# Optimization experiments

Measured on AMD Instinct MI355X. Metric: run time of the kernel, lower is better.

## Reference

```python
import jax, jax.numpy as jnp
import numpy as np

HIDDEN = 1024
NHEAD = 16
HEAD_DIM = HIDDEN // NHEAD
B, S = 2, 2048


def setup_inputs() -> dict:
    key = jax.random.key(0)
    ks = jax.random.split(key, 10)
    scale = 1.0 / np.sqrt(HIDDEN)
    inp = {
        "x": jax.random.normal(ks[0], (B, S, HIDDEN), dtype=jnp.float32),
        "mask": jax.random.randint(ks[1], (B, S), 0, 2).astype(bool),
        "Wq": jax.random.normal(ks[2], (HIDDEN, HIDDEN), dtype=jnp.float32) * scale,
        "bq": jnp.zeros((HIDDEN,), dtype=jnp.float32),
        "Wk": jax.random.normal(ks[3], (HIDDEN, HIDDEN), dtype=jnp.float32) * scale,
        "bk": jnp.zeros((HIDDEN,), dtype=jnp.float32),
        "Wv": jax.random.normal(ks[4], (HIDDEN, HIDDEN), dtype=jnp.float32) * scale,
        "bv": jnp.zeros((HIDDEN,), dtype=jnp.float32),
        "Wo": jax.random.normal(ks[5], (HIDDEN, HIDDEN), dtype=jnp.float32) * scale,
        "bo": jnp.zeros((HIDDEN,), dtype=jnp.float32),
    }
    return inp


def reference(x, mask, Wq, bq, Wk, bk, Wv, bv, Wo, bo):
    B_, S_, H = x.shape
    # QKV projections (torch Linear: x @ W.T + b), split into heads -> [B, nhead, S, head_dim]
    def split_heads(t):
        return t.reshape(B_, S_, NHEAD, HEAD_DIM).transpose(0, 2, 1, 3)

    q = split_heads(x @ Wq.T + bq)
    k = split_heads(x @ Wk.T + bk)
    v = split_heads(x @ Wv.T + bv)

    # scaled dot-product scores: [B, nhead, S, S]
    energy = jnp.einsum("bhqd,bhkd->bhqk", q, k) / jnp.sqrt(jnp.float32(HEAD_DIM))

    # combined padding + diagonal-exclusion mask: mask keys where mask[b,k] is True,
    # but never mask the diagonal (self) position
    eye = jnp.eye(S_, dtype=bool)  # [S, S]
    attn_mask = mask[:, None, None, :] & ~eye[None, None, :, :]  # [B, 1, S, S] broadcast over heads
    energy = jnp.where(attn_mask, -jnp.inf, energy)

    attention = jax.nn.softmax(energy, axis=-1)
    out = jnp.einsum("bhqk,bhkd->bhqd", attention, v)  # [B, nhead, S, head_dim]
    out = out.transpose(0, 2, 1, 3).reshape(B_, S_, H)
    return out @ Wo.T + bo
```

## Files before the change

kernel.cpp:

```cpp
#include <hip/hip_runtime.h>

typedef __attribute__((ext_vector_type(8))) short short8;
typedef __attribute__((ext_vector_type(4))) float f32x4;
typedef __attribute__((ext_vector_type(16))) float f32x16;
typedef __attribute__((ext_vector_type(4))) unsigned short ushort4v;

#define HIDDEN 1024
#define NHEAD 16
#define HD 64
#define BATCH 2
#define SEQ 2048
#define MROWS (BATCH * SEQ)
#define QSCALE 0.18033688011112042f

__device__ __forceinline__ unsigned short f2b(float f) {
  union { float f; unsigned u; } v; v.f = f;
  unsigned r = v.u + 0x7fffu + ((v.u >> 16) & 1u);
  return (unsigned short)(r >> 16);
}

__device__ __forceinline__ unsigned cvt_pk_bf16(float lo, float hi) {
  unsigned r;
  asm("v_cvt_pk_bf16_f32 %0, %1, %2" : "=v"(r) : "v"(lo), "v"(hi));
  return r;
}

__device__ __forceinline__ float fexp2(float x) {
#if __has_builtin(__builtin_amdgcn_exp2f)
  return __builtin_amdgcn_exp2f(x);
#else
  return exp2f(x);
#endif
}

__device__ __forceinline__ void gll16(const void* g, void* l) {
  __builtin_amdgcn_global_load_lds(
      (__attribute__((address_space(1))) void*)g,
      (__attribute__((address_space(3))) void*)l, 16, 0, 0);
}

__global__ void prep_kernel(const float* __restrict__ x,
                            const float* __restrict__ Wq,
                            const float* __restrict__ Wk,
                            const float* __restrict__ Wv,
                            const float* __restrict__ Wo,
                            unsigned short* __restrict__ xb,
                            unsigned short* __restrict__ wqb,
                            unsigned short* __restrict__ wkb,
                            unsigned short* __restrict__ wvb,
                            unsigned short* __restrict__ wob) {
  int bid = blockIdx.x;
  const float* src;
  unsigned short* dst;
  int base;
  if (bid < 4096)      { src = x;  dst = xb;  base = bid; }
  else if (bid < 5120) { src = Wq; dst = wqb; base = bid - 4096; }
  else if (bid < 6144) { src = Wk; dst = wkb; base = bid - 5120; }
  else if (bid < 7168) { src = Wv; dst = wvb; base = bid - 6144; }
  else                 { src = Wo; dst = wob; base = bid - 7168; }
  int i = (base * 256 + threadIdx.x) * 4;
  float4 v = *reinterpret_cast<const float4*>(src + i);
  ushort4v o;
  o.x = f2b(v.x); o.y = f2b(v.y); o.z = f2b(v.z); o.w = f2b(v.w);
  *reinterpret_cast<ushort4v*>(dst + i) = o;
}

__global__ void amask_kernel(const int* __restrict__ m, float* __restrict__ am,
                             int n) {
  int i = blockIdx.x * blockDim.x + threadIdx.x;
  if (i < n) am[i] = m[i] ? -1e30f : 0.f;
}

__global__ __launch_bounds__(256) void gemm_qkv_kernel(
    const unsigned short* __restrict__ A,
    const unsigned short* __restrict__ W0,
    const unsigned short* __restrict__ W1,
    const unsigned short* __restrict__ W2,
    const float* __restrict__ c0, const float* __restrict__ c1,
    const float* __restrict__ c2, void* __restrict__ o0,
    void* __restrict__ o1, void* __restrict__ o2) {
  __shared__ __align__(16) unsigned short Al[2][64 * 64];
  __shared__ __align__(16) unsigned short Bl[2][128 * 64];
  const int t = threadIdx.x;
  const int w = t >> 6, l = t & 63;
  const int hi = l >> 4, lo16 = l & 15;
  const int m0 = blockIdx.x * 64;
  const int n0 = blockIdx.y * 128;
  const int K = HIDDEN;

  const int region = n0 >> 10;
  const int n_loc = n0 & 1023;
  const unsigned short* Bsel = region == 0 ? W0 : (region == 1 ? W1 : W2);
  const float* bias = region == 0 ? c0 : (region == 1 ? c1 : c2);

  const int schunk = (l & 7) ^ (l >> 3);
  const int rsw = (lo16 & 7);

  const unsigned short* pA[2];
#pragma unroll
  for (int i = 0; i < 2; ++i)
    pA[i] = A + (size_t)(m0 + w * 16 + i * 8 + (l >> 3)) * K + schunk * 8;
  const unsigned short* pB[4];
#pragma unroll
  for (int i = 0; i < 4; ++i)
    pB[i] = Bsel + (size_t)(n_loc + w * 32 + i * 8 + (l >> 3)) * K + schunk * 8;

  f32x4 acc[4][2];
#pragma unroll
  for (int mi = 0; mi < 4; ++mi)
#pragma unroll
    for (int f = 0; f < 2; ++f) acc[mi][f] = f32x4{0.f, 0.f, 0.f, 0.f};

  auto stage = [&](int BUF) __attribute__((always_inline)) {
#pragma unroll
    for (int i = 0; i < 2; ++i) {
      gll16(pA[i], &Al[BUF][(w * 16 + i * 8) * 64]);
      pA[i] += 64;
    }
#pragma unroll
    for (int i = 0; i < 4; ++i) {
      gll16(pB[i], &Bl[BUF][(w * 32 + i * 8) * 64]);
      pB[i] += 64;
    }
  };

  stage(0);
  __syncthreads();

  auto step = [&](int knext, int BUF) __attribute__((always_inline)) {
    if (knext < K) stage(BUF ^ 1);
#pragma unroll
    for (int kk = 0; kk < 2; ++kk) {
      short8 af[4], bf[2];
#pragma unroll
      for (int mi = 0; mi < 4; ++mi)
        af[mi] = *reinterpret_cast<const short8*>(
            &Al[BUF][(mi * 16 + lo16) * 64 + (((kk * 4 + hi) ^ rsw) * 8)]);
#pragma unroll
      for (int f = 0; f < 2; ++f)
        bf[f] = *reinterpret_cast<const short8*>(
            &Bl[BUF][(w * 32 + f * 16 + lo16) * 64 + (((kk * 4 + hi) ^ rsw) * 8)]);
#pragma unroll
      for (int mi = 0; mi < 4; ++mi)
#pragma unroll
        for (int f = 0; f < 2; ++f)
          acc[mi][f] =
              __builtin_amdgcn_mfma_f32_16x16x32_bf16(af[mi], bf[f], acc[mi][f], 0, 0, 0);
    }
    __syncthreads();
  };

  for (int kt = 0; kt < K; kt += 128) {
    step(kt + 64, 0);
    step(kt + 128, 1);
  }

#pragma unroll
  for (int mi = 0; mi < 4; ++mi)
#pragma unroll
    for (int f = 0; f < 2; ++f) {
      int mbase = m0 + mi * 16 + hi * 4;
      int n_rel = n_loc + w * 32 + f * 16 + lo16;
      float bv_ = bias[n_rel];
      if (region == 2) {
        int b = mbase >> 11, s = mbase & 2047, d = n_rel & 63, h = n_rel >> 6;
        uint2 pk;
        pk.x = cvt_pk_bf16(acc[mi][f][0] + bv_, acc[mi][f][1] + bv_);
        pk.y = cvt_pk_bf16(acc[mi][f][2] + bv_, acc[mi][f][3] + bv_);
        *reinterpret_cast<uint2*>(
            (unsigned short*)o2 + ((size_t)(b * NHEAD + h) * HD + d) * SEQ + s) = pk;
        continue;
      }
#pragma unroll
      for (int j = 0; j < 4; ++j) {
        float v = acc[mi][f][j] + bv_;
        int mm = mbase + j;
        int b = mm >> 11, s = mm & 2047, h = n_rel >> 6, d = n_rel & 63;
        if (region == 0)
          ((unsigned short*)o0)[((size_t)(b * NHEAD + h) * SEQ + s) * HD + d] =
              f2b(v * QSCALE);
        else
          ((unsigned short*)o1)[((size_t)(b * NHEAD + h) * SEQ + s) * HD + d] =
              f2b(v);
      }
    }
}

__global__ __launch_bounds__(256) void gemm_o_kernel(
    const unsigned short* __restrict__ A, const unsigned short* __restrict__ W0,
    const float* __restrict__ bias, float* __restrict__ out) {
  __shared__ __align__(16) unsigned short Al[2][64 * 64];
  __shared__ __align__(16) unsigned short Bl[2][128 * 64];
  const int t = threadIdx.x;
  const int w = t >> 6, l = t & 63;
  const int hi = l >> 4, lo16 = l & 15;
  const int m0 = blockIdx.x * 64;
  const int n0 = blockIdx.y * 128;
  const int K = HIDDEN;

  const int schunk = (l & 7) ^ (l >> 3);
  const int rsw = (lo16 & 7);

  const unsigned short* pA[2];
#pragma unroll
  for (int i = 0; i < 2; ++i)
    pA[i] = A + (size_t)(m0 + w * 16 + i * 8 + (l >> 3)) * K + schunk * 8;
  const unsigned short* pB[4];
#pragma unroll
  for (int i = 0; i < 4; ++i)
    pB[i] = W0 + (size_t)(n0 + w * 32 + i * 8 + (l >> 3)) * K + schunk * 8;

  f32x4 acc[4][2];
#pragma unroll
  for (int mi = 0; mi < 4; ++mi)
#pragma unroll
    for (int f = 0; f < 2; ++f) acc[mi][f] = f32x4{0.f, 0.f, 0.f, 0.f};

  auto stage = [&](int BUF) __attribute__((always_inline)) {
#pragma unroll
    for (int i = 0; i < 2; ++i) {
      gll16(pA[i], &Al[BUF][(w * 16 + i * 8) * 64]);
      pA[i] += 64;
    }
#pragma unroll
    for (int i = 0; i < 4; ++i) {
      gll16(pB[i], &Bl[BUF][(w * 32 + i * 8) * 64]);
      pB[i] += 64;
    }
  };

  stage(0);
  __syncthreads();

  auto step = [&](int knext, int BUF) __attribute__((always_inline)) {
    if (knext < K) stage(BUF ^ 1);
#pragma unroll
    for (int kk = 0; kk < 2; ++kk) {
      short8 af[4], bf[2];
#pragma unroll
      for (int mi = 0; mi < 4; ++mi)
        af[mi] = *reinterpret_cast<const short8*>(
            &Al[BUF][(mi * 16 + lo16) * 64 + (((kk * 4 + hi) ^ rsw) * 8)]);
#pragma unroll
      for (int f = 0; f < 2; ++f)
        bf[f] = *reinterpret_cast<const short8*>(
            &Bl[BUF][(w * 32 + f * 16 + lo16) * 64 + (((kk * 4 + hi) ^ rsw) * 8)]);
#pragma unroll
      for (int mi = 0; mi < 4; ++mi)
#pragma unroll
        for (int f = 0; f < 2; ++f)
          acc[mi][f] =
              __builtin_amdgcn_mfma_f32_16x16x32_bf16(af[mi], bf[f], acc[mi][f], 0, 0, 0);
    }
    __syncthreads();
  };

  for (int kt = 0; kt < K; kt += 128) {
    step(kt + 64, 0);
    step(kt + 128, 1);
  }

#pragma unroll
  for (int mi = 0; mi < 4; ++mi)
#pragma unroll
    for (int f = 0; f < 2; ++f) {
      int mbase = m0 + mi * 16 + hi * 4;
      int n = n0 + w * 32 + f * 16 + lo16;
      float bv_ = bias[n];
#pragma unroll
      for (int j = 0; j < 4; ++j)
        out[(size_t)(mbase + j) * HIDDEN + n] = acc[mi][f][j] + bv_;
    }
}

__global__ __launch_bounds__(512) void attn_kernel(
    const unsigned short* __restrict__ Q, const unsigned short* __restrict__ Km,
    const unsigned short* __restrict__ Vt, const float* __restrict__ amf,
    unsigned short* __restrict__ O) {
  __shared__ __align__(16) unsigned short KV[4][2][64 * 64];
  __shared__ float SrwS[4][64];
  const int t = threadIdx.x;
  const int w = t >> 6, l = t & 63;
  const int q31 = l & 31, hi32 = l >> 5;
  const int qg = w >> 1, half = w & 1;
  const int nb = ((blockIdx.x & 7) << 6) | (blockIdx.x >> 3);
  const int qt = nb & 15, bh = nb >> 4;
  const int b = bh >> 4, h = bh & 15;
  const int q0w = qt * 128 + qg * 32;
  const int q = q0w + q31;
  const bool diagw = (half == (qg & 1));
  const int dtile = qt * 128 + (qg >> 1) * 64;

  const unsigned short* Qb = Q + (size_t)bh * SEQ * HD;
  const unsigned short* Kb = Km + (size_t)bh * SEQ * HD;
  const unsigned short* Vb = Vt + (size_t)bh * HD * SEQ;
  const float* mb = amf + b * SEQ + half * 32;

  short8 qf[4];
#pragma unroll
  for (int dc = 0; dc < 4; ++dc)
    qf[dc] = *reinterpret_cast<const short8*>(
        Qb + (size_t)q * HD + dc * 16 + hi32 * 8);

  f32x16 o0, o1;
#pragma unroll
  for (int r = 0; r < 16; ++r) { o0[r] = 0.f; o1[r] = 0.f; }
  float srw = 0.f;

  const int srow = w * 8 + (l >> 3);
  const int sc_ = ((l & 7) ^ (l >> 3) ^ (w & 3)) * 8;
  const unsigned short* pK = Kb + (size_t)srow * HD + sc_;
  const unsigned short* pV = Vb + (size_t)srow * SEQ + sc_;

  auto stageT = [&](int BUF) __attribute__((always_inline)) {
    gll16(pK, &KV[BUF][0][(w * 8) * 64]);
    gll16(pV, &KV[BUF][1][(w * 8) * 64]);
    pK += 64 * HD; pV += 64;
  };

  stageT(0);
  stageT(1);
  stageT(2);
  asm volatile("s_waitcnt vmcnt(4)" ::: "memory");
  __builtin_amdgcn_s_barrier();
  __builtin_amdgcn_sched_barrier(0);

  const int rk = (q31 & 7) ^ (q31 >> 3);

  auto step = [&](int k0, int BUF, int NBUF, int WAITN) __attribute__((always_inline)) {
    float4 a0[4];
#pragma unroll
    for (int g = 0; g < 4; ++g)
      a0[g] = *reinterpret_cast<const float4*>(mb + k0 + g * 8 + hi32 * 4);

    if (k0 + 192 < SEQ) stageT(NBUF);

    f32x16 s0;
    if (diagw && k0 == dtile) {
      int kb = hi32 * 4;
#pragma unroll
      for (int g = 0; g < 4; ++g) {
        if (kb + g * 8 + 0 == q31) a0[g].x = 0.f;
        if (kb + g * 8 + 1 == q31) a0[g].y = 0.f;
        if (kb + g * 8 + 2 == q31) a0[g].z = 0.f;
        if (kb + g * 8 + 3 == q31) a0[g].w = 0.f;
      }
    }
#pragma unroll
    for (int g = 0; g < 4; ++g) {
      s0[4 * g + 0] = a0[g].x; s0[4 * g + 1] = a0[g].y;
      s0[4 * g + 2] = a0[g].z; s0[4 * g + 3] = a0[g].w;
    }

    __builtin_amdgcn_s_setprio(1);
#pragma unroll
    for (int dc = 0; dc < 4; ++dc) {
      short8 kf = *reinterpret_cast<const short8*>(
          &KV[BUF][0][(half * 32 + q31) * 64 + (((dc * 2 + hi32) ^ rk) * 8)]);
      s0 = __builtin_amdgcn_mfma_f32_32x32x16_bf16(kf, qf[dc], s0, 0, 0, 0);
    }
    __builtin_amdgcn_s_setprio(0);

    float sum = 0.f;
#pragma unroll
    for (int r = 0; r < 16; ++r) {
      float p = fexp2(s0[r]);
      s0[r] = p;
      sum += p;
    }
    {
      unsigned a = __float_as_uint(sum), bsw = a;
      auto rr = __builtin_amdgcn_permlane32_swap(a, bsw, false, false);
      sum = __uint_as_float(rr[0]) + __uint_as_float(rr[1]);
    }
    srw += sum;

    unsigned c[8];
#pragma unroll
    for (int R = 0; R < 4; ++R) {
      c[R * 2 + 0] = cvt_pk_bf16(s0[4 * R + 0], s0[4 * R + 1]);
      c[R * 2 + 1] = cvt_pk_bf16(s0[4 * R + 2], s0[4 * R + 3]);
    }

    short8 pb[2];
#pragma unroll
    for (int sl = 0; sl < 2; ++sl) {
      const int R0 = sl * 2;
      auto r0 = __builtin_amdgcn_permlane32_swap(c[R0 * 2 + 0],
                                                 c[(R0 + 1) * 2 + 0], false, false);
      auto r1 = __builtin_amdgcn_permlane32_swap(c[R0 * 2 + 1],
                                                 c[(R0 + 1) * 2 + 1], false, false);
      union { unsigned u[4]; short8 s8; } pu;
      pu.u[0] = r0[0]; pu.u[1] = r1[0]; pu.u[2] = r0[1]; pu.u[3] = r1[1];
      pb[sl] = pu.s8;
    }

    __builtin_amdgcn_s_setprio(1);
#pragma unroll
    for (int sl = 0; sl < 2; ++sl) {
      int ch = (((half * 2 + sl) * 2 + hi32) ^ rk) * 8;
      short8 vf0 = *reinterpret_cast<const short8*>(&KV[BUF][1][q31 * 64 + ch]);
      short8 vf1 =
          *reinterpret_cast<const short8*>(&KV[BUF][1][(32 + q31) * 64 + ch]);
      o0 = __builtin_amdgcn_mfma_f32_32x32x16_bf16(vf0, pb[sl], o0, 0, 0, 0);
      o1 = __builtin_amdgcn_mfma_f32_32x32x16_bf16(vf1, pb[sl], o1, 0, 0, 0);
    }
    __builtin_amdgcn_s_setprio(0);

    if (WAITN == 4)
      asm volatile("s_waitcnt vmcnt(4)" ::: "memory");
    else if (WAITN == 2)
      asm volatile("s_waitcnt vmcnt(2)" ::: "memory");
    else if (WAITN == 0)
      asm volatile("s_waitcnt vmcnt(0)" ::: "memory");
    if (WAITN >= 0) {
      __builtin_amdgcn_s_barrier();
      __builtin_amdgcn_sched_barrier(0);
    }
  };

  for (int tt = 0; tt < 28; tt += 4) {
    step((tt + 0) * 64, 0, 3, 4);
    step((tt + 1) * 64, 1, 0, 4);
    step((tt + 2) * 64, 2, 1, 4);
    step((tt + 3) * 64, 3, 2, 4);
  }
  step(28 * 64, 0, 3, 4);
  step(29 * 64, 1, 0, 2);
  step(30 * 64, 2, 1, 0);
  step(31 * 64, 3, 2, -1);

  float* obuf = (float*)&KV[0][0][0];
  if (half) {
    float* d = obuf + (qg * 64 + l) * 33;
#pragma unroll
    for (int r = 0; r < 16; ++r) { d[r] = o0[r]; d[16 + r] = o1[r]; }
    SrwS[qg][l] = srw;
  }
  __syncthreads();
  if (!half) {
    const float* d = obuf + (qg * 64 + l) * 33;
#pragma unroll
    for (int r = 0; r < 16; ++r) { o0[r] += d[r]; o1[r] += d[16 + r]; }
    srw += SrwS[qg][l];

    float rinv = 1.f / srw;
    unsigned short* Ob = O + (size_t)(b * SEQ + q) * HIDDEN + h * HD;
#pragma unroll
    for (int g = 0; g < 4; ++g) {
      uint2 w0, w1;
      w0.x = cvt_pk_bf16(o0[4 * g + 0] * rinv, o0[4 * g + 1] * rinv);
      w0.y = cvt_pk_bf16(o0[4 * g + 2] * rinv, o0[4 * g + 3] * rinv);
      w1.x = cvt_pk_bf16(o1[4 * g + 0] * rinv, o1[4 * g + 1] * rinv);
      w1.y = cvt_pk_bf16(o1[4 * g + 2] * rinv, o1[4 * g + 3] * rinv);
      *reinterpret_cast<uint2*>(Ob + 8 * g + 4 * hi32) = w0;
      *reinterpret_cast<uint2*>(Ob + 32 + 8 * g + 4 * hi32) = w1;
    }
  }
}

extern "C" void kernel_launch(void* const* d_in, const int* in_sizes, int n_in,
                              void* d_out, int out_size, void* d_ws,
                              size_t ws_size, hipStream_t stream) {
  const float* x = (const float*)d_in[0];
  const int* mask = (const int*)d_in[1];
  const float* Wq = (const float*)d_in[2];
  const float* bq = (const float*)d_in[3];
  const float* Wk = (const float*)d_in[4];
  const float* bk = (const float*)d_in[5];
  const float* Wv = (const float*)d_in[6];
  const float* bv = (const float*)d_in[7];
  const float* Wo = (const float*)d_in[8];
  const float* bo = (const float*)d_in[9];

  char* ws = (char*)d_ws;
  unsigned short* xb  = (unsigned short*)(ws + ((size_t)0 << 20));
  unsigned short* wqb = (unsigned short*)(ws + ((size_t)8 << 20));
  unsigned short* wkb = (unsigned short*)(ws + ((size_t)10 << 20));
  unsigned short* wvb = (unsigned short*)(ws + ((size_t)12 << 20));
  unsigned short* wob = (unsigned short*)(ws + ((size_t)14 << 20));
  unsigned short* qw  = (unsigned short*)(ws + ((size_t)16 << 20));
  unsigned short* kw  = (unsigned short*)(ws + ((size_t)24 << 20));
  unsigned short* vtw = (unsigned short*)(ws + ((size_t)32 << 20));
  unsigned short* ow  = (unsigned short*)(ws + ((size_t)40 << 20));
  float* amf = (float*)(ws + ((size_t)0 << 20));

  prep_kernel<<<8192, 256, 0, stream>>>(x, Wq, Wk, Wv, Wo, xb, wqb, wkb, wvb,
                                        wob);

  gemm_qkv_kernel<<<dim3(MROWS / 64, 3 * HIDDEN / 128), 256, 0, stream>>>(
      xb, wqb, wkb, wvb, bq, bk, bv, qw, kw, vtw);

  amask_kernel<<<MROWS / 256, 256, 0, stream>>>(mask, amf, MROWS);

  attn_kernel<<<512, 512, 0, stream>>>(qw, kw, vtw, amf, ow);

  gemm_o_kernel<<<dim3(MROWS / 64, HIDDEN / 128), 256, 0, stream>>>(
      ow, wob, bo, (float*)d_out);
}
```

Measured before the change: 115.1 us.

## Software-pipeline QK^T of the next tile with softmax and PV of the current

Splits the attention inner step into a QK^T phase and a softmax+PV phase, then issues the next tile's QK^T MFMAs before the current tile's exp, pack and PV work, using two alternating score registers. Each prefetch wait is tightened to one tile ahead so the next K tile is resident before its QK^T runs. The aim is to overlap MFMA latency with the VALU exp/convert work. It costs an extra 16-float accumulator per lane, which raises register pressure, and it shortens the load lookahead.

```diff
diff --git a/kernel.cpp b/kernel.cpp
--- a/kernel.cpp
+++ b/kernel.cpp
@@ -321,21 +321,17 @@
   stageT(0);
   stageT(1);
   stageT(2);
-  asm volatile("s_waitcnt vmcnt(4)" ::: "memory");
+  asm volatile("s_waitcnt vmcnt(2)" ::: "memory");
   __builtin_amdgcn_s_barrier();
   __builtin_amdgcn_sched_barrier(0);
 
   const int rk = (q31 & 7) ^ (q31 >> 3);
 
-  auto step = [&](int k0, int BUF, int NBUF, int WAITN) __attribute__((always_inline)) {
+  auto qk = [&](int k0, int BUF, f32x16& s) __attribute__((always_inline)) {
     float4 a0[4];
 #pragma unroll
     for (int g = 0; g < 4; ++g)
       a0[g] = *reinterpret_cast<const float4*>(mb + k0 + g * 8 + hi32 * 4);
-
-    if (k0 + 192 < SEQ) stageT(NBUF);
-
-    f32x16 s0;
     if (diagw && k0 == dtile) {
       int kb = hi32 * 4;
 #pragma unroll
@@ -348,24 +344,25 @@
     }
 #pragma unroll
     for (int g = 0; g < 4; ++g) {
-      s0[4 * g + 0] = a0[g].x; s0[4 * g + 1] = a0[g].y;
-      s0[4 * g + 2] = a0[g].z; s0[4 * g + 3] = a0[g].w;
-    }
-
+      s[4 * g + 0] = a0[g].x; s[4 * g + 1] = a0[g].y;
+      s[4 * g + 2] = a0[g].z; s[4 * g + 3] = a0[g].w;
+    }
     __builtin_amdgcn_s_setprio(1);
 #pragma unroll
     for (int dc = 0; dc < 4; ++dc) {
       short8 kf = *reinterpret_cast<const short8*>(
           &KV[BUF][0][(half * 32 + q31) * 64 + (((dc * 2 + hi32) ^ rk) * 8)]);
-      s0 = __builtin_amdgcn_mfma_f32_32x32x16_bf16(kf, qf[dc], s0, 0, 0, 0);
+      s = __builtin_amdgcn_mfma_f32_32x32x16_bf16(kf, qf[dc], s, 0, 0, 0);
     }
     __builtin_amdgcn_s_setprio(0);
-
+  };
+
+  auto spv = [&](int BUF, f32x16& s) __attribute__((always_inline)) {
     float sum = 0.f;
 #pragma unroll
     for (int r = 0; r < 16; ++r) {
-      float p = fexp2(s0[r]);
-      s0[r] = p;
+      float p = fexp2(s[r]);
+      s[r] = p;
       sum += p;
     }
     {
@@ -378,8 +375,8 @@
     unsigned c[8];
 #pragma unroll
     for (int R = 0; R < 4; ++R) {
-      c[R * 2 + 0] = cvt_pk_bf16(s0[4 * R + 0], s0[4 * R + 1]);
-      c[R * 2 + 1] = cvt_pk_bf16(s0[4 * R + 2], s0[4 * R + 3]);
+      c[R * 2 + 0] = cvt_pk_bf16(s[4 * R + 0], s[4 * R + 1]);
+      c[R * 2 + 1] = cvt_pk_bf16(s[4 * R + 2], s[4 * R + 3]);
     }
 
     short8 pb[2];
@@ -406,10 +403,17 @@
       o1 = __builtin_amdgcn_mfma_f32_32x32x16_bf16(vf1, pb[sl], o1, 0, 0, 0);
     }
     __builtin_amdgcn_s_setprio(0);
-
-    if (WAITN == 4)
-      asm volatile("s_waitcnt vmcnt(4)" ::: "memory");
-    else if (WAITN == 2)
+  };
+
+  f32x16 sA, sB;
+  qk(0, 0, sA);
+
+  auto pipe = [&](int k0, int BUF, int NBUF, f32x16& scur, f32x16& snext,
+                  int WAITN) __attribute__((always_inline)) {
+    if (k0 + 192 < SEQ) stageT(NBUF);
+    if (k0 + 64 < SEQ) qk(k0 + 64, (BUF + 1) & 3, snext);
+    spv(BUF, scur);
+    if (WAITN == 2)
       asm volatile("s_waitcnt vmcnt(2)" ::: "memory");
     else if (WAITN == 0)
       asm volatile("s_waitcnt vmcnt(0)" ::: "memory");
@@ -420,15 +424,15 @@
   };
 
   for (int tt = 0; tt < 28; tt += 4) {
-    step((tt + 0) * 64, 0, 3, 4);
-    step((tt + 1) * 64, 1, 0, 4);
-    step((tt + 2) * 64, 2, 1, 4);
-    step((tt + 3) * 64, 3, 2, 4);
+    pipe((tt + 0) * 64, 0, 3, sA, sB, 2);
+    pipe((tt + 1) * 64, 1, 0, sB, sA, 2);
+    pipe((tt + 2) * 64, 2, 1, sA, sB, 2);
+    pipe((tt + 3) * 64, 3, 2, sB, sA, 2);
   }
-  step(28 * 64, 0, 3, 4);
-  step(29 * 64, 1, 0, 2);
-  step(30 * 64, 2, 1, 0);
-  step(31 * 64, 3, 2, -1);
+  pipe(28 * 64, 0, 3, sA, sB, 2);
+  pipe(29 * 64, 1, 0, sB, sA, 0);
+  pipe(30 * 64, 2, 1, sA, sB, -1);
+  pipe(31 * 64, 3, 2, sB, sA, -1);
 
   float* obuf = (float*)&KV[0][0][0];
   if (half) {
```

New measurement: 114.5 us (median of 2 runs). Within noise of the previous version (-0.6%).
